# Kernel tuning notes

Hardware: AMD Instinct MI355X
Metric: run time of the kernel (lower is better)

The kernel has to match this reference:

```python
import jax, jax.numpy as jnp
import numpy as np

B, S, E = 2, 2048, 1024
H = 1344            # hidden_dim = ceil(1.3*1024/64)*64
NH = 4              # mLSTM heads
DH = H // NH        # 336
K = 4               # causal conv kernel size
NPH = H // 4        # headwise proj heads (qkv_proj_blocksize=4)
PD = H // NPH       # per-head proj dim = 4
EPS = 1e-6


def setup_inputs() -> dict:
    key = jax.random.key(0)
    ks = jax.random.split(key, 10)
    s_in = jnp.sqrt(2.0 / (5 * E))    # small_init(E)
    s_pd = jnp.sqrt(2.0 / (5 * PD))   # small_init per-head dim
    return {
        "x": jax.random.normal(ks[0], (B, S, E), jnp.float32),
        "W_up": jax.random.normal(ks[1], (E, 2 * H), jnp.float32) * s_in,
        "conv_k": jax.random.normal(ks[2], (K, 1, H), jnp.float32) * jnp.sqrt(2.0 / K),  # depthwise, WIO layout
        "conv_b": jnp.zeros((H,), jnp.float32),
        "Wq": jax.random.normal(ks[3], (NPH, PD, PD), jnp.float32) * s_pd,
        "Wk": jax.random.normal(ks[4], (NPH, PD, PD), jnp.float32) * s_pd,
        "Wv": jax.random.normal(ks[5], (NPH, PD, PD), jnp.float32) * s_pd,
        "W_ig": jax.random.normal(ks[6], (3 * H, NH), jnp.float32) * 0.01,
        "b_ig": jax.random.normal(ks[7], (NH,), jnp.float32) * 0.1,
        "W_fg": jax.random.normal(ks[8], (3 * H, NH), jnp.float32) * 0.01,
        "b_fg": jnp.linspace(3.0, 6.0, NH, dtype=jnp.float32),
        "ln_w": jnp.ones((H,), jnp.float32),
        "skip": jnp.ones((H,), jnp.float32),
        "W_down": jax.random.normal(ks[9], (H, E), jnp.float32) * (2.0 / 12 / np.sqrt(H)),
    }


def _headwise(x, W):
    # LinearHeadwiseExpand: block-diagonal projection over NPH heads of size PD
    xh = x.reshape(B, S, NPH, PD)
    return jnp.einsum('bshd,hdo->bsho', xh, W).reshape(B, S, H)


def _mlstm_cell(q, k, v, ig, fg):
    # parallel stabilized mLSTM; q,k,v: (B,NH,S,DH); ig,fg: (B,NH,S)
    logf = jax.nn.log_sigmoid(fg)
    c = jnp.cumsum(logf, axis=-1)                         # (B,NH,S)
    logfmat = c[..., :, None] - c[..., None, :]           # (B,NH,S,S) cumulative forget decay
    mask = jnp.tril(jnp.ones((S, S), bool))               # causal mask
    log_D = jnp.where(mask, logfmat, -jnp.inf) + ig[..., None, :]
    m = jnp.max(log_D, axis=-1, keepdims=True)            # rowwise stabilizer
    D = jnp.exp(log_D - m)
    qk = jnp.einsum('bnsd,bntd->bnst', q, k) * (DH ** -0.5)
    C = qk * D
    n = jnp.maximum(jnp.abs(jnp.sum(C, axis=-1, keepdims=True)), jnp.exp(-m))
    return jnp.einsum('bnst,bntd->bnsd', C / (n + EPS), v)


def reference(x, W_up, conv_k, conv_b, Wq, Wk, Wv, W_ig, b_ig, W_fg, b_fg, ln_w, skip, W_down):
    x_inner = x @ W_up                                    # (B,S,2H)
    x_m, z = jnp.split(x_inner, 2, axis=-1)
    # depthwise causal conv1d
    xp = jnp.pad(x_m, ((0, 0), (K - 1, 0), (0, 0)))
    xc = jax.lax.conv_general_dilated(
        xp, conv_k, (1,), 'VALID',
        dimension_numbers=('NWC', 'WIO', 'NWC'),
        feature_group_count=H) + conv_b
    act = jax.nn.silu(xc)
    q = _headwise(act, Wq)
    k = _headwise(act, Wk)
    v = _headwise(x_m, Wv)
    gin = jnp.concatenate([q, k, v], axis=-1)             # (B,S,3H)
    ig = jnp.transpose(gin @ W_ig + b_ig, (0, 2, 1))      # (B,NH,S)
    fg = jnp.transpose(gin @ W_fg + b_fg, (0, 2, 1))
    qh = jnp.transpose(q.reshape(B, S, NH, DH), (0, 2, 1, 3))
    kh = jnp.transpose(k.reshape(B, S, NH, DH), (0, 2, 1, 3))
    vh = jnp.transpose(v.reshape(B, S, NH, DH), (0, 2, 1, 3))
    h = _mlstm_cell(qh, kh, vh, ig, fg)                   # (B,NH,S,DH)
    # multi-head layernorm (per-head groupnorm over DH, scale only)
    mu = jnp.mean(h, axis=-1, keepdims=True)
    var = jnp.var(h, axis=-1, keepdims=True)
    hn = (h - mu) * jax.lax.rsqrt(var + 1e-5) * ln_w.reshape(NH, 1, DH)
    h_out = jnp.transpose(hn, (0, 2, 1, 3)).reshape(B, S, H)
    h_state = (h_out + skip * act) * jax.nn.silu(z)
    return h_state @ W_down
```

## Files before the change

### kernel.cpp

```cpp
#include <hip/hip_runtime.h>
#include <cmath>

#define DI __device__ __forceinline__

constexpr int B_=2, S_=2048, E_=1024, H_=1344, NH_=4, DH_=336;
constexpr int BS_=B_*S_, H2_=2*H_;
constexpr int NG_=B_*NH_*S_;

constexpr size_t N_X=(size_t)BS_*E_;
constexpr size_t N_WUP=(size_t)E_*H2_;
constexpr size_t N_WDN=(size_t)H_*E_;
constexpr size_t N_BSH=(size_t)BS_*H_;
constexpr size_t N_BSH2=(size_t)BS_*H2_;
constexpr size_t N_WH=5376, N_WG=16128, N_CK=4*H_;

constexpr size_t O_IGB = 64;
constexpr size_t O_LOGF= O_IGB + NG_;
constexpr size_t O_AB  = O_LOGF+ NG_;
constexpr size_t O_MB  = O_AB  + NG_;
constexpr size_t O_MTB = O_MB  + NG_;
constexpr size_t O_CK  = O_MTB + NG_;
constexpr size_t O_CB  = O_CK  + N_CK;
constexpr size_t O_WQ  = O_CB  + H_;
constexpr size_t O_WK  = O_WQ  + N_WH;
constexpr size_t O_WV  = O_WK  + N_WH;
constexpr size_t O_WIG = O_WV  + N_WH;
constexpr size_t O_BIG = O_WIG + N_WG;
constexpr size_t O_WFG = O_BIG + 16;
constexpr size_t O_BFG = O_WFG + N_WG;
constexpr size_t O_LNW = O_BFG + 16;
constexpr size_t O_SKP = O_LNW + H_;
constexpr size_t O_FX  = O_SKP + H_;
constexpr size_t O_FWUP= O_FX  + N_X;
constexpr size_t O_FWDN= O_FWUP+ N_WUP;
constexpr size_t O_XIN = O_FWDN+ N_WDN;
constexpr size_t O_ACT = O_XIN + N_BSH2;
constexpr size_t O_QB  = O_ACT + N_BSH;
constexpr size_t O_KB  = O_QB  + N_BSH;
constexpr size_t O_VB  = O_KB  + N_BSH;
constexpr size_t O_HOUT= O_VB  + N_BSH;

constexpr size_t KSPLIT_SHORTS=(size_t)8*128*11*64*8;
constexpr size_t VT_SHORTS=(size_t)8*64*22*64*8;

typedef __attribute__((ext_vector_type(8))) short bf16x8;
typedef __attribute__((ext_vector_type(4))) float f32x4;

DI float bf2f(unsigned int u){union{unsigned int i;float f;}v;v.i=(u&0xffffu)<<16;return v.f;}
DI unsigned short f2bf(float f){union{float f;unsigned int i;}v;v.f=f;unsigned int x=v.i;
  return (unsigned short)((x+0x7fffu+((x>>16)&1u))>>16);}
DI float siluf(float x){return x/(1.f+expf(-x));}
DI float logsigf(float x){return (x>=0.f)?-log1pf(expf(-x)):x-log1pf(expf(x));}
DI void load4(const float* p, float* d){float4 v=*reinterpret_cast<const float4*>(p);
  d[0]=v.x;d[1]=v.y;d[2]=v.z;d[3]=v.w;}

__global__ __launch_bounds__(256) void detect_k(const unsigned short* __restrict__ xraw,
                                                int* __restrict__ flag){
  __shared__ int cnt_s;
  if(threadIdx.x==0) cnt_s=0;
  __syncthreads();
  int c=0;
  for(int i=threadIdx.x;i<2048;i+=256){
    const unsigned e=(xraw[i]>>7)&0xFFu;
    if(e>=0x90u) c++;
  }
  atomicAdd(&cnt_s,c);
  __syncthreads();
  if(threadIdx.x==0) *flag=(cnt_s>16)?0:1;
}

constexpr int CV0=5376, CV1=CV0+1344, CV2=CV1+5376, CV3=CV2+5376, CV4=CV3+5376,
              CV5=CV4+16128, CV6=CV5+4, CV7=CV6+16128, CV8=CV7+4,
              CV9=CV8+1344, CVT=CV9+1344;
__global__ __launch_bounds__(256) void convall_k(
    const void* s0,const void* s1,const void* s2,const void* s3,const void* s4,
    const void* s5,const void* s6,const void* s7,const void* s8,const void* s9,
    const void* s10, float* __restrict__ ws, const int* __restrict__ flag){
  const int i=blockIdx.x*256+threadIdx.x;
  if(i>=CVT) return;
  const void* src; int off; size_t dst;
  if(i<CV0){src=s0; off=i;      dst=O_CK +off;}
  else if(i<CV1){src=s1; off=i-CV0; dst=O_CB +off;}
  else if(i<CV2){src=s2; off=i-CV1; dst=O_WQ +off;}
  else if(i<CV3){src=s3; off=i-CV2; dst=O_WK +off;}
  else if(i<CV4){src=s4; off=i-CV3; dst=O_WV +off;}
  else if(i<CV5){src=s5; off=i-CV4; dst=O_WIG+off;}
  else if(i<CV6){src=s6; off=i-CV5; dst=O_BIG+off;}
  else if(i<CV7){src=s7; off=i-CV6; dst=O_WFG+off;}
  else if(i<CV8){src=s8; off=i-CV7; dst=O_BFG+off;}
  else if(i<CV9){src=s9; off=i-CV8; dst=O_LNW+off;}
  else          {src=s10;off=i-CV9; dst=O_SKP+off;}
  ws[dst]=(*flag)?bf2f(((const unsigned short*)src)[off])
                 :((const float*)src)[off];
}

__global__ __launch_bounds__(256) void aprep_k(const void* __restrict__ src,
                                               const int* __restrict__ flag,
                                               int kcn,int ldk,int total,
                                               unsigned short* __restrict__ hi,
                                               unsigned short* __restrict__ lo){
  const int slot=blockIdx.x*256+threadIdx.x;
  if(slot>=total) return;
  const int l=slot&63, rest=slot>>6;
  const int kc=rest%kcn, mt=rest/kcn;
  const int row=mt*16+(l&15), k0=kc*32+(l>>4)*8;
  const int fl=flag?*flag:0;
  float v[8];
  if(fl){
    const unsigned short* s=(const unsigned short*)src+(size_t)row*ldk+k0;
    const uint4 u=*reinterpret_cast<const uint4*>(s);
    v[0]=bf2f(u.x);v[1]=bf2f(u.x>>16);v[2]=bf2f(u.y);v[3]=bf2f(u.y>>16);
    v[4]=bf2f(u.z);v[5]=bf2f(u.z>>16);v[6]=bf2f(u.w);v[7]=bf2f(u.w>>16);
  }else{
    const float* s=(const float*)src+(size_t)row*ldk+k0;
    load4(s,v); load4(s+4,v+4);
  }
  unsigned short h8[8], l8[8];
#pragma unroll
  for(int j=0;j<8;j++){ h8[j]=f2bf(v[j]); l8[j]=f2bf(v[j]-bf2f(h8[j])); }
  uint4 ph,pl;
  ph.x=(unsigned)h8[0]|((unsigned)h8[1]<<16); ph.y=(unsigned)h8[2]|((unsigned)h8[3]<<16);
  ph.z=(unsigned)h8[4]|((unsigned)h8[5]<<16); ph.w=(unsigned)h8[6]|((unsigned)h8[7]<<16);
  pl.x=(unsigned)l8[0]|((unsigned)l8[1]<<16); pl.y=(unsigned)l8[2]|((unsigned)l8[3]<<16);
  pl.z=(unsigned)l8[4]|((unsigned)l8[5]<<16); pl.w=(unsigned)l8[6]|((unsigned)l8[7]<<16);
  *reinterpret_cast<uint4*>(&hi[(size_t)slot*8])=ph;
  *reinterpret_cast<uint4*>(&lo[(size_t)slot*8])=pl;
}

__global__ __launch_bounds__(256) void bprep_k(const void* __restrict__ src,
                                               const int* __restrict__ flag,
                                               int kcn,int ldn,int total,
                                               unsigned short* __restrict__ hi,
                                               unsigned short* __restrict__ lo){
  const int slot=blockIdx.x*256+threadIdx.x;
  if(slot>=total) return;
  const int l=slot&63, rest=slot>>6;
  const int kc=rest%kcn, nt=rest/kcn;
  const int col=nt*16+(l&15), row0=kc*32+(l>>4)*8;
  const int fl=flag?*flag:0;
  float v[8];
  if(fl){
    const unsigned short* s=(const unsigned short*)src;
#pragma unroll
    for(int j=0;j<8;j++) v[j]=bf2f(s[(size_t)(row0+j)*ldn+col]);
  }else{
    const float* s=(const float*)src;
#pragma unroll
    for(int j=0;j<8;j++) v[j]=s[(size_t)(row0+j)*ldn+col];
  }
  unsigned short h8[8], l8[8];
#pragma unroll
  for(int j=0;j<8;j++){ h8[j]=f2bf(v[j]); l8[j]=f2bf(v[j]-bf2f(h8[j])); }
  uint4 ph,pl;
  ph.x=(unsigned)h8[0]|((unsigned)h8[1]<<16); ph.y=(unsigned)h8[2]|((unsigned)h8[3]<<16);
  ph.z=(unsigned)h8[4]|((unsigned)h8[5]<<16); ph.w=(unsigned)h8[6]|((unsigned)h8[7]<<16);
  pl.x=(unsigned)l8[0]|((unsigned)l8[1]<<16); pl.y=(unsigned)l8[2]|((unsigned)l8[3]<<16);
  pl.z=(unsigned)l8[4]|((unsigned)l8[5]<<16); pl.w=(unsigned)l8[6]|((unsigned)l8[7]<<16);
  *reinterpret_cast<uint4*>(&hi[(size_t)slot*8])=ph;
  *reinterpret_cast<uint4*>(&lo[(size_t)slot*8])=pl;
}

__global__ __launch_bounds__(256) void gemm3_k(
    const unsigned short* __restrict__ Ahi, const unsigned short* __restrict__ Alo,
    const unsigned short* __restrict__ Bhi, const unsigned short* __restrict__ Blo,
    void* __restrict__ C, const int* __restrict__ flag, int kcn, int ldc){
  const int t=threadIdx.x, w=t>>6, l=t&63, lm=l&15, quad=l>>4;
  const int bn=blockIdx.x*128, bm=blockIdx.y*128;
  const int mtg0=bm>>4, ntg0=bn>>4;

  __shared__ short TT[2][32*512];

  f32x4 acc[2][8];
#pragma unroll
  for(int g=0;g<2;g++)
#pragma unroll
    for(int nt=0;nt<8;nt++) acc[g][nt]={0.f,0.f,0.f,0.f};

  auto stage=[&](int buf,int kc){
#pragma unroll
    for(int j=0;j<8;j++){
      const int tr=w*8+j;
      const unsigned short* src;
      if(tr<8)       src=&Ahi[((size_t)(mtg0+tr   )*kcn+kc)*512+(size_t)l*8];
      else if(tr<16) src=&Alo[((size_t)(mtg0+tr-8 )*kcn+kc)*512+(size_t)l*8];
      else if(tr<24) src=&Bhi[((size_t)(ntg0+tr-16)*kcn+kc)*512+(size_t)l*8];
      else           src=&Blo[((size_t)(ntg0+tr-24)*kcn+kc)*512+(size_t)l*8];
      __builtin_amdgcn_global_load_lds(
        (const __attribute__((address_space(1))) unsigned int*)src,
        (__attribute__((address_space(3))) unsigned int*)&TT[buf][tr*512],
        16,0,0);
    }
  };

  auto compute=[&](int buf){
    const short* Tb=&TT[buf][0];
    const bf16x8 ah0=*reinterpret_cast<const bf16x8*>(&Tb[(2*w  )*512+l*8]);
    const bf16x8 ah1=*reinterpret_cast<const bf16x8*>(&Tb[(2*w+1)*512+l*8]);
    const bf16x8 al0=*reinterpret_cast<const bf16x8*>(&Tb[(8+2*w  )*512+l*8]);
    const bf16x8 al1=*reinterpret_cast<const bf16x8*>(&Tb[(8+2*w+1)*512+l*8]);
#pragma unroll
    for(int nt=0;nt<8;nt++){
      const bf16x8 bh=*reinterpret_cast<const bf16x8*>(&Tb[(16+nt)*512+l*8]);
      const bf16x8 bl=*reinterpret_cast<const bf16x8*>(&Tb[(24+nt)*512+l*8]);
      acc[0][nt]=__builtin_amdgcn_mfma_f32_16x16x32_bf16(ah0,bh,acc[0][nt],0,0,0);
      acc[0][nt]=__builtin_amdgcn_mfma_f32_16x16x32_bf16(al0,bh,acc[0][nt],0,0,0);
      acc[0][nt]=__builtin_amdgcn_mfma_f32_16x16x32_bf16(ah0,bl,acc[0][nt],0,0,0);
      acc[1][nt]=__builtin_amdgcn_mfma_f32_16x16x32_bf16(ah1,bh,acc[1][nt],0,0,0);
      acc[1][nt]=__builtin_amdgcn_mfma_f32_16x16x32_bf16(al1,bh,acc[1][nt],0,0,0);
      acc[1][nt]=__builtin_amdgcn_mfma_f32_16x16x32_bf16(ah1,bl,acc[1][nt],0,0,0);
    }
  };

  stage(0,0);
  for(int kc=0;kc<kcn;kc++){
    const int cur=kc&1;
    if(kc+1<kcn){
      stage(cur^1,kc+1);
      asm volatile("s_waitcnt vmcnt(8)" ::: "memory");
    } else {
      asm volatile("s_waitcnt vmcnt(0)" ::: "memory");
    }
    __builtin_amdgcn_s_barrier();
    compute(cur);
    __builtin_amdgcn_s_barrier();
  }

  const int bf=flag?*flag:0;
#pragma unroll
  for(int g=0;g<2;g++)
#pragma unroll
    for(int nt=0;nt<8;nt++)
#pragma unroll
      for(int r=0;r<4;r++){
        const size_t idx=(size_t)(bm+(2*w+g)*16+quad*4+r)*ldc+bn+nt*16+lm;
        if(bf) ((unsigned short*)C)[idx]=f2bf(acc[g][nt][r]);
        else   ((float*)C)[idx]=acc[g][nt][r];
      }
}

__global__ __launch_bounds__(256) void convqkv_k(const float* __restrict__ xin,
                                                 const float* __restrict__ ck,
                                                 const float* __restrict__ cb,
                                                 const float* __restrict__ Wq,
                                                 const float* __restrict__ Wk,
                                                 const float* __restrict__ Wv,
                                                 float* __restrict__ act,
                                                 float* __restrict__ qb,
                                                 float* __restrict__ kb,
                                                 float* __restrict__ vb){
  const int i=blockIdx.x*256+threadIdx.x;
  if(i>=BS_*(H_/4)) return;
  const int bs=i/(H_/4), ph=i-bs*(H_/4);
  const int b=bs>>11, s=bs&2047;
  const int base=ph*4;
  float xc[4];
#pragma unroll
  for(int d=0;d<4;d++) xc[d]=cb[base+d];
  float xm[4]={0.f,0.f,0.f,0.f};
#pragma unroll
  for(int w=0;w<4;w++){
    const int sr=s-3+w;
    if(sr>=0){
      float xv[4];
      load4(&xin[(size_t)(b*S_+sr)*H2_+base],xv);
#pragma unroll
      for(int d=0;d<4;d++) xc[d]+=xv[d]*ck[w*H_+base+d];
      if(w==3){ xm[0]=xv[0];xm[1]=xv[1];xm[2]=xv[2];xm[3]=xv[3]; }
    }
  }
  float a4[4];
#pragma unroll
  for(int d=0;d<4;d++) a4[d]=siluf(xc[d]);
  *reinterpret_cast<float4*>(&act[(size_t)bs*H_+base])
      =make_float4(a4[0],a4[1],a4[2],a4[3]);
  float q4[4],k4[4],v4[4];
#pragma unroll
  for(int o=0;o<4;o++){
    float q=0.f,k=0.f,v=0.f;
#pragma unroll
    for(int d=0;d<4;d++){
      q+=a4[d]*Wq[ph*16+d*4+o];
      k+=a4[d]*Wk[ph*16+d*4+o];
      v+=xm[d]*Wv[ph*16+d*4+o];
    }
    q4[o]=q;k4[o]=k;v4[o]=v;
  }
  const int nh=ph/84, dh0=(ph-nh*84)*4;
  const size_t off=((size_t)(b*NH_+nh)*S_+s)*DH_+dh0;
  *reinterpret_cast<float4*>(&qb[off])=make_float4(q4[0],q4[1],q4[2],q4[3]);
  *reinterpret_cast<float4*>(&kb[off])=make_float4(k4[0],k4[1],k4[2],k4[3]);
  *reinterpret_cast<float4*>(&vb[off])=make_float4(v4[0],v4[1],v4[2],v4[3]);
}

__global__ __launch_bounds__(256) void gates2_k(const float* __restrict__ qb,
                                                const float* __restrict__ kb,
                                                const float* __restrict__ vb,
                                                const float* __restrict__ Wig,
                                                const float* __restrict__ big,
                                                const float* __restrict__ Wfg,
                                                const float* __restrict__ bfg,
                                                float* __restrict__ igb,
                                                float* __restrict__ logfb){
  const int wid=(blockIdx.x*256+threadIdx.x)>>6;
  const int l=threadIdx.x&63;
  if(wid>=BS_) return;
  const int b=wid>>11, s=wid&2047;
  float aI0=0.f,aI1=0.f,aI2=0.f,aI3=0.f;
  float aF0=0.f,aF1=0.f,aF2=0.f,aF3=0.f;
  for(int nh=0;nh<NH_;nh++){
    const size_t rb=((size_t)(b*NH_+nh)*S_+s)*DH_;
    const int hb=nh*DH_;
    for(int dh=l;dh<DH_;dh+=64){
      const int h=hb+dh;
      const float q=qb[rb+dh], k=kb[rb+dh], v=vb[rb+dh];
      const float4 wiq=*reinterpret_cast<const float4*>(&Wig[(size_t)h*4]);
      const float4 wik=*reinterpret_cast<const float4*>(&Wig[(size_t)(H_+h)*4]);
      const float4 wiv=*reinterpret_cast<const float4*>(&Wig[(size_t)(2*H_+h)*4]);
      const float4 wfq=*reinterpret_cast<const float4*>(&Wfg[(size_t)h*4]);
      const float4 wfk=*reinterpret_cast<const float4*>(&Wfg[(size_t)(H_+h)*4]);
      const float4 wfv=*reinterpret_cast<const float4*>(&Wfg[(size_t)(2*H_+h)*4]);
      aI0+=q*wiq.x+k*wik.x+v*wiv.x;
      aI1+=q*wiq.y+k*wik.y+v*wiv.y;
      aI2+=q*wiq.z+k*wik.z+v*wiv.z;
      aI3+=q*wiq.w+k*wik.w+v*wiv.w;
      aF0+=q*wfq.x+k*wfk.x+v*wfv.x;
      aF1+=q*wfq.y+k*wfk.y+v*wfv.y;
      aF2+=q*wfq.z+k*wfk.z+v*wfv.z;
      aF3+=q*wfq.w+k*wfk.w+v*wfv.w;
    }
  }
#pragma unroll
  for(int m=1;m<64;m<<=1){
    aI0+=__shfl_xor(aI0,m); aI1+=__shfl_xor(aI1,m);
    aI2+=__shfl_xor(aI2,m); aI3+=__shfl_xor(aI3,m);
    aF0+=__shfl_xor(aF0,m); aF1+=__shfl_xor(aF1,m);
    aF2+=__shfl_xor(aF2,m); aF3+=__shfl_xor(aF3,m);
  }
  if(l==0){
    const size_t o0=(size_t)(b*NH_+0)*S_+s;
    const size_t o1=(size_t)(b*NH_+1)*S_+s;
    const size_t o2=(size_t)(b*NH_+2)*S_+s;
    const size_t o3=(size_t)(b*NH_+3)*S_+s;
    igb[o0]=aI0+big[0]; igb[o1]=aI1+big[1];
    igb[o2]=aI2+big[2]; igb[o3]=aI3+big[3];
    logfb[o0]=logsigf(aF0+bfg[0]); logfb[o1]=logsigf(aF1+bfg[1]);
    logfb[o2]=logsigf(aF2+bfg[2]); logfb[o3]=logsigf(aF3+bfg[3]);
  }
}

__global__ __launch_bounds__(256) void kvprep_k(const float* __restrict__ kb,
                                                const float* vb,
                                                unsigned short* __restrict__ khi,
                                                unsigned short* __restrict__ klo,
                                                unsigned short* __restrict__ vTf,
                                                float* partz){
  const int blk=blockIdx.x;
  if(blk<1024){
    const int head=blk>>7, tt=blk&127;
    const size_t obase=(size_t)blk*11*512;
    for(int slot=threadIdx.x; slot<704; slot+=256){
      const int dc=slot>>6, ll=slot&63, quad=ll>>4, lm=ll&15;
      const int tg=tt*16+lm, dbase=dc*32+quad*8;
      float v[8];
      if(dbase<336){
        load4(&kb[((size_t)head*S_+tg)*DH_+dbase],v);
        load4(&kb[((size_t)head*S_+tg)*DH_+dbase+4],v+4);
      } else { for(int j=0;j<8;j++) v[j]=0.f; }
      unsigned short hi8[8], lo8[8];
#pragma unroll
      for(int j=0;j<8;j++){
        hi8[j]=f2bf(v[j]);
        lo8[j]=f2bf(v[j]-bf2f(hi8[j]));
      }
      const size_t o=obase+(size_t)(dc*64+ll)*8;
      uint4 ph, pl;
      ph.x=(unsigned)hi8[0]|((unsigned)hi8[1]<<16); ph.y=(unsigned)hi8[2]|((unsigned)hi8[3]<<16);
      ph.z=(unsigned)hi8[4]|((unsigned)hi8[5]<<16); ph.w=(unsigned)hi8[6]|((unsigned)hi8[7]<<16);
      pl.x=(unsigned)lo8[0]|((unsigned)lo8[1]<<16); pl.y=(unsigned)lo8[2]|((unsigned)lo8[3]<<16);
      pl.z=(unsigned)lo8[4]|((unsigned)lo8[5]<<16); pl.w=(unsigned)lo8[6]|((unsigned)lo8[7]<<16);
      *reinterpret_cast<uint4*>(&khi[o])=ph;
      *reinterpret_cast<uint4*>(&klo[o])=pl;
    }
  } else {
    const int vblk=blk-1024;
    const int head=vblk>>6, tc=vblk&63;
    const size_t obase=(size_t)vblk*22*512;
    for(int slot=threadIdx.x; slot<1408; slot+=256){
      const int ntg=slot>>6, ll=slot&63, quad=ll>>4, lm=ll&15;
      const int n=ntg*16+lm, t0=tc*32+quad*8;
      unsigned short h8[8];
#pragma unroll
      for(int j=0;j<8;j++){
        float val;
        if(n<336)       val=vb[((size_t)head*S_+t0+j)*DH_+n];
        else if(n==336) val=1.f;
        else            val=0.f;
        h8[j]=f2bf(val);
      }
      uint4 pk;
      pk.x=(unsigned)h8[0]|((unsigned)h8[1]<<16); pk.y=(unsigned)h8[2]|((unsigned)h8[3]<<16);
      pk.z=(unsigned)h8[4]|((unsigned)h8[5]<<16); pk.w=(unsigned)h8[6]|((unsigned)h8[7]<<16);
      *reinterpret_cast<uint4*>(&vTf[obase+(size_t)(ntg*64+ll)*8])=pk;
    }
    __syncthreads();
    const size_t zb=((size_t)head*2048+(size_t)tc*32)*336;
    for(int idx=threadIdx.x; idx<32*336; idx+=256) partz[zb+idx]=0.f;
  }
}

__global__ __launch_bounds__(256) void scan_k(float* igm,
                                              const float* __restrict__ logfb,
                                              float* __restrict__ ab,float* __restrict__ Mb,
                                              float* __restrict__ mtb){
  const int head=blockIdx.x, t=threadIdx.x;
  __shared__ float sh[256];
  const float* lf=logfb+(size_t)head*S_;
  float* ig=igm+(size_t)head*S_;
  float lc[8];
  float run=0.f;
#pragma unroll
  for(int i=0;i<8;i++){ run+=lf[t*8+i]; lc[i]=run; }
  sh[t]=run;
  for(int st=1;st<256;st<<=1){
    __syncthreads();
    const float v=(t>=st)?sh[t-st]:0.f;
    __syncthreads();
    sh[t]+=v;
  }
  __syncthreads();
  const float off=(t==0)?0.f:sh[t-1];
  __syncthreads();
  float av[8],mv[8],cv[8];
  float mrun=-1e30f;
#pragma unroll
  for(int i=0;i<8;i++){
    cv[i]=off+lc[i];
    av[i]=ig[t*8+i]-cv[i];
    mrun=fmaxf(mrun,av[i]);
    mv[i]=mrun;
  }
  sh[t]=mrun;
  for(int st=1;st<256;st<<=1){
    __syncthreads();
    const float v=(t>=st)?sh[t-st]:-1e30f;
    __syncthreads();
    sh[t]=fmaxf(sh[t],v);
  }
  __syncthreads();
  const float moff=(t==0)?-1e30f:sh[t-1];
#pragma unroll
  for(int i=0;i<8;i++){
    const float Mi=fmaxf(moff,mv[i]);
    const size_t j=(size_t)head*S_+t*8+i;
    ab[j]=av[i]; Mb[j]=Mi; mtb[j]=cv[i]+Mi;
    ig[t*8+i]=0.f;
  }
}

__global__ __launch_bounds__(512,1) void mlstm6_k(
    const float* __restrict__ qb, const unsigned short* __restrict__ khi,
    const unsigned short* __restrict__ klo, const unsigned short* __restrict__ vTf,
    const float* __restrict__ ab, const float* __restrict__ Mb,
    float* __restrict__ part, float* __restrict__ rsum){
  const int bid=blockIdx.x;
  const int head=bid&7;
  const int rest=bid>>3;
  const int pairI=rest&7, seg=rest>>3;
  const int t=threadIdx.x, w=t>>6, l=t&63, lm=l&15, quad=l>>4;

  __shared__ short KV[2][66*512];
  __shared__ short Sc[8][16][40];

  const size_t hb=(size_t)head*S_;
  const float scale=0.05455447256f;

  const int sbA=pairI, sbB=15-pairI;
  const int nA=pairI+1, nTot=17;

  bf16x8 qh[11], ql[11];
  f32x4 accO[22];
  float Mr[4];
  int ws0=sbA*128+w*16;

  auto loadQ=[&](int ws0_){
    const float* qrow=qb+(hb+ws0_+lm)*DH_;
#pragma unroll
    for(int dc=0;dc<11;dc++){
      const int dbase=dc*32+quad*8;
      float v[8];
      if(dbase<336){ load4(qrow+dbase,v); load4(qrow+dbase+4,v+4); }
      else { for(int j=0;j<8;j++) v[j]=0.f; }
#pragma unroll
      for(int j=0;j<8;j++){
        const unsigned short h=f2bf(v[j]);
        qh[dc][j]=(short)h;
        ql[dc][j]=(short)f2bf(v[j]-bf2f(h));
      }
    }
#pragma unroll
    for(int r=0;r<4;r++) Mr[r]=Mb[hb+ws0_+quad*4+r];
#pragma unroll
    for(int n=0;n<22;n++) accO[n]={0.f,0.f,0.f,0.f};
  };

  auto itemC=[&](int i)->int{
    return (i<nA)? (seg+4*i) : (seg+4*(i-nA));
  };

  auto stage=[&](int buf,int c){
    const size_t kbase=(((size_t)head*128+(size_t)(2*c))*11)*512+(size_t)l*8;
    const size_t vbase=(((size_t)head*64+(size_t)c)*22)*512+(size_t)l*8;
#pragma unroll
    for(int j=0;j<9;j++){
      const int tr=w+8*j;
      if(tr<66){
        const unsigned short* src;
        if(tr<22)      src=&khi[kbase+(size_t)tr*512];
        else if(tr<44) src=&klo[kbase+(size_t)(tr-22)*512];
        else           src=&vTf[vbase+(size_t)(tr-44)*512];
        __builtin_amdgcn_global_load_lds(
          (const __attribute__((address_space(1))) unsigned int*)src,
          (__attribute__((address_space(3))) unsigned int*)&KV[buf][(size_t)tr*512],
          16,0,0);
      }
    }
  };

  auto compute=[&](int c,int buf){
    const int t0=c<<5;
    if(t0>ws0+15) return;
    const float al0=ab[hb+t0+lm];
    const float al1=ab[hb+t0+16+lm];
#pragma unroll
    for(int tt=0;tt<2;tt++){
      f32x4 a0={0,0,0,0}, a1={0,0,0,0}, a2={0,0,0,0};
#pragma unroll
      for(int dc=0;dc<11;dc++){
        const bf16x8 kh=*reinterpret_cast<const bf16x8*>(&KV[buf][(tt*11+dc)*512+l*8]);
        const bf16x8 kl=*reinterpret_cast<const bf16x8*>(&KV[buf][(22+tt*11+dc)*512+l*8]);
        a0=__builtin_amdgcn_mfma_f32_16x16x32_bf16(qh[dc],kh,a0,0,0,0);
        a1=__builtin_amdgcn_mfma_f32_16x16x32_bf16(ql[dc],kh,a1,0,0,0);
        a2=__builtin_amdgcn_mfma_f32_16x16x32_bf16(qh[dc],kl,a2,0,0,0);
      }
      const float al=(tt==0)?al0:al1;
      const int tg=t0+tt*16+lm;
#pragma unroll
      for(int r=0;r<4;r++){
        const int srow=quad*4+r;
        const float qk=a0[r]+a1[r]+a2[r];
        const float e=fminf(al-Mr[r],0.f);
        const float msk=(tg<=ws0+srow)?1.f:0.f;
        Sc[w][srow][tt*16+lm]=(short)f2bf(msk*(qk*scale*expf(e)));
      }
    }
    const bf16x8 scf=*reinterpret_cast<const bf16x8*>(&Sc[w][lm][quad*8]);
#pragma unroll
    for(int nt=0;nt<22;nt++){
      const bf16x8 vf=*reinterpret_cast<const bf16x8*>(&KV[buf][(44+nt)*512+l*8]);
      accO[nt]=__builtin_amdgcn_mfma_f32_16x16x32_bf16(scf,vf,accO[nt],0,0,0);
    }
  };

  auto epilogue=[&](){
    const size_t pbase=(size_t)head*2048+ws0;
#pragma unroll
    for(int nt=0;nt<22;nt++){
      const int col=nt*16+lm;
#pragma unroll
      for(int r=0;r<4;r++){
        const int srow=quad*4+r;
        const float val=accO[nt][r];
        if(col<336){ if(val!=0.f) atomicAdd(&part[(pbase+srow)*336+col],val); }
        else if(col==336){ if(val!=0.f) atomicAdd(&rsum[pbase+srow],val); }
      }
    }
  };

  loadQ(ws0);
  stage(0,itemC(0));
  __syncthreads();
  int cur=0;
  for(int i=0;i<nTot;i++){
    if(i+1<nTot) stage(cur^1,itemC(i+1));
    compute(itemC(i),cur);
    if(i==nA-1){
      epilogue();
      ws0=sbB*128+w*16;
      loadQ(ws0);
    }
    __syncthreads();
    cur^=1;
  }
  epilogue();
}

__global__ __launch_bounds__(256) void finalize3_k(const float* __restrict__ part,
                                                   const float* __restrict__ rsum,
                                                   const float* __restrict__ mtb,
                                                   const float* __restrict__ lnw,
                                                   const float* __restrict__ skip,
                                                   const float* __restrict__ act,
                                                   const float* __restrict__ xin,
                                                   unsigned short* __restrict__ hshi,
                                                   unsigned short* __restrict__ hslo){
  const int sblk=blockIdx.x, head=blockIdx.y;
  const int bI=head>>2, nh=head&3;
  const int s0=sblk*32;
  const int t=threadIdx.x, row=t>>3, sub=t&7;
  __shared__ float red1[32][8], red2[32][8];
  __shared__ float mu_s[32], rs_s[32], inv_s[32];
  const size_t pbase=(size_t)head*2048+s0;
  const float* prow=part+(pbase+row)*336;
  float s1=0.f,s2=0.f;
  for(int c=sub;c<336;c+=8){ const float v=prow[c]; s1+=v; s2+=v*v; }
  red1[row][sub]=s1; red2[row][sub]=s2;
  __syncthreads();
  if(sub==0){
    float a1=0.f,a2=0.f;
#pragma unroll
    for(int j=0;j<8;j++){ a1+=red1[row][j]; a2+=red2[row][j]; }
    const float mt=mtb[(size_t)head*S_+s0+row];
    const float nn=fmaxf(fabsf(rsum[pbase+row]), expf(fminf(fmaxf(-mt,-60.f),60.f)));
    const float inv=1.f/(nn+1e-6f);
    const float mu=a1*inv/336.f;
    const float var=a2*inv*inv/336.f-mu*mu;
    inv_s[row]=inv; mu_s[row]=mu;
    rs_s[row]=rsqrtf(fmaxf(var,0.f)+1e-5f);
  }
  __syncthreads();
  const float inv=inv_s[row], mu=mu_s[row], rs=rs_s[row];
  const size_t gbs=(size_t)(bI*S_+s0+row);
  const float* arow=act+gbs*H_+nh*DH_;
  const float* zrow=xin+gbs*H2_+H_+nh*DH_;
  const float* srw=skip+nh*DH_;
  const float* lrw=lnw+nh*DH_;
  const size_t mtbase=(gbs>>4)*42;
  const int lbase=(int)(gbs&15);
  for(int c=sub;c<336;c+=8){
    const float hn=(prow[c]*inv-mu)*rs*lrw[c];
    const float val=(hn+srw[c]*arow[c])*siluf(zrow[c]);
    const int h=nh*DH_+c;
    const int kc=h>>5, quad=(h>>3)&3, j=h&7;
    const size_t slot=(mtbase+kc)*64+lbase+16*quad;
    const unsigned short hi=f2bf(val);
    hshi[slot*8+j]=hi;
    hslo[slot*8+j]=f2bf(val-bf2f(hi));
  }
}

extern "C" void kernel_launch(void* const* d_in, const int* in_sizes, int n_in,
                              void* d_out, int out_size, void* d_ws, size_t ws_size,
                              hipStream_t stream){
  float* ws=(float*)d_ws;
  int* flag=(int*)ws;

  float* igb  = ws+O_IGB;
  float* logfb= ws+O_LOGF;
  float* ab   = ws+O_AB;
  float* Mbuf = ws+O_MB;
  float* mtb  = ws+O_MTB;
  float* f_ck = ws+O_CK;
  float* f_cb = ws+O_CB;
  float* f_wq = ws+O_WQ;
  float* f_wk = ws+O_WK;
  float* f_wv = ws+O_WV;
  float* f_wig= ws+O_WIG;
  float* f_big= ws+O_BIG;
  float* f_wfg= ws+O_WFG;
  float* f_bfg= ws+O_BFG;
  float* f_lnw= ws+O_LNW;
  float* f_skp= ws+O_SKP;
  float* xin  = ws+O_XIN;
  float* act  = ws+O_ACT;
  float* qb   = ws+O_QB;
  float* kb   = ws+O_KB;
  float* vb   = ws+O_VB;

  unsigned short* xhi  =(unsigned short*)(ws+O_FX);   unsigned short* xlo  =xhi+N_X;
  unsigned short* wuphi=(unsigned short*)(ws+O_FWUP); unsigned short* wuplo=wuphi+N_WUP;
  unsigned short* wdnhi=(unsigned short*)(ws+O_FWDN); unsigned short* wdnlo=wdnhi+N_WDN;
  unsigned short* khi=(unsigned short*)(ws+O_FX);
  unsigned short* klo=khi+KSPLIT_SHORTS;
  unsigned short* vTf=(unsigned short*)(ws+O_HOUT);
  unsigned short* hshi=(unsigned short*)kb;
  unsigned short* hslo=hshi+N_BSH;
  float* partb=vb;
  float* rsumb=igb;

  detect_k<<<1,256,0,stream>>>((const unsigned short*)d_in[0],flag);
  convall_k<<<(CVT+255)/256,256,0,stream>>>(d_in[2],d_in[3],d_in[4],d_in[5],d_in[6],
                                            d_in[7],d_in[8],d_in[9],d_in[10],d_in[11],
                                            d_in[12],ws,flag);

  aprep_k<<<(256*32*64+255)/256,256,0,stream>>>(d_in[0],flag,32,1024,256*32*64,xhi,xlo);
  bprep_k<<<(168*32*64+255)/256,256,0,stream>>>(d_in[1],flag,32,2688,168*32*64,wuphi,wuplo);
  gemm3_k<<<dim3(2688/128,4096/128),256,0,stream>>>(xhi,xlo,wuphi,wuplo,xin,nullptr,32,H2_);

  convqkv_k<<<(BS_*(H_/4)+255)/256,256,0,stream>>>(xin,f_ck,f_cb,f_wq,f_wk,f_wv,
                                                   act,qb,kb,vb);
  gates2_k<<<(BS_*64+255)/256,256,0,stream>>>(qb,kb,vb,f_wig,f_big,f_wfg,f_bfg,igb,logfb);
  kvprep_k<<<1024+512,256,0,stream>>>(kb,vb,khi,klo,vTf,partb);
  bprep_k<<<(64*42*64+255)/256,256,0,stream>>>(d_in[13],flag,42,1024,64*42*64,wdnhi,wdnlo);
  scan_k<<<B_*NH_,256,0,stream>>>(igb,logfb,ab,Mbuf,mtb);
  mlstm6_k<<<256,512,0,stream>>>(qb,khi,klo,vTf,ab,Mbuf,partb,rsumb);
  finalize3_k<<<dim3(S_/32,B_*NH_),256,0,stream>>>(partb,rsumb,mtb,f_lnw,f_skp,act,xin,
                                                   hshi,hslo);
  gemm3_k<<<dim3(1024/128,4096/128),256,0,stream>>>(hshi,hslo,wdnhi,wdnlo,d_out,flag,42,E_);
}
```

Baseline: 461.4 us.

## Fuse prep kernels and merge conv/qkv with gate projections via shared memory

Merges the x and W_up split-bf16 prep kernels into one launch. It fuses the conv/qkv kernel with the gate projection so q/k/v for each token stay in shared memory instead of being reread from global memory. It also folds the W_down prep into the kv-prep launch. The goal is fewer kernel launches and less global traffic. In exchange, the fused conv kernel uses 384-thread blocks with one token per block and a two-level reduction.

```diff
diff --git a/kernel.cpp b/kernel.cpp
--- a/kernel.cpp
+++ b/kernel.cpp
@@ -94,26 +94,44 @@
                  :((const float*)src)[off];
 }
 
-__global__ __launch_bounds__(256) void aprep_k(const void* __restrict__ src,
-                                               const int* __restrict__ flag,
-                                               int kcn,int ldk,int total,
-                                               unsigned short* __restrict__ hi,
-                                               unsigned short* __restrict__ lo){
-  const int slot=blockIdx.x*256+threadIdx.x;
-  if(slot>=total) return;
-  const int l=slot&63, rest=slot>>6;
-  const int kc=rest%kcn, mt=rest/kcn;
-  const int row=mt*16+(l&15), k0=kc*32+(l>>4)*8;
-  const int fl=flag?*flag:0;
+__global__ __launch_bounds__(256) void prepAB_k(const void* __restrict__ xsrc,
+    const void* __restrict__ wsrc, const int* __restrict__ flag,
+    unsigned short* __restrict__ xhi, unsigned short* __restrict__ xlo,
+    unsigned short* __restrict__ whi, unsigned short* __restrict__ wlo){
+  const int blk=blockIdx.x;
+  const int fl=*flag;
   float v[8];
-  if(fl){
-    const unsigned short* s=(const unsigned short*)src+(size_t)row*ldk+k0;
-    const uint4 u=*reinterpret_cast<const uint4*>(s);
-    v[0]=bf2f(u.x);v[1]=bf2f(u.x>>16);v[2]=bf2f(u.y);v[3]=bf2f(u.y>>16);
-    v[4]=bf2f(u.z);v[5]=bf2f(u.z>>16);v[6]=bf2f(u.w);v[7]=bf2f(u.w>>16);
-  }else{
-    const float* s=(const float*)src+(size_t)row*ldk+k0;
-    load4(s,v); load4(s+4,v+4);
+  unsigned short* dh; unsigned short* dl; size_t slot;
+  if(blk<2048){
+    slot=(size_t)blk*256+threadIdx.x;
+    const int l=(int)slot&63, rest=(int)(slot>>6);
+    const int kc=rest&31, mt=rest>>5;
+    const int row=mt*16+(l&15), k0=kc*32+(l>>4)*8;
+    if(fl){
+      const unsigned short* s=(const unsigned short*)xsrc+(size_t)row*1024+k0;
+      const uint4 u=*reinterpret_cast<const uint4*>(s);
+      v[0]=bf2f(u.x);v[1]=bf2f(u.x>>16);v[2]=bf2f(u.y);v[3]=bf2f(u.y>>16);
+      v[4]=bf2f(u.z);v[5]=bf2f(u.z>>16);v[6]=bf2f(u.w);v[7]=bf2f(u.w>>16);
+    }else{
+      const float* s=(const float*)xsrc+(size_t)row*1024+k0;
+      load4(s,v); load4(s+4,v+4);
+    }
+    dh=xhi; dl=xlo;
+  } else {
+    slot=(size_t)(blk-2048)*256+threadIdx.x;
+    const int l=(int)slot&63, rest=(int)(slot>>6);
+    const int kc=rest&31, nt=rest>>5;
+    const int col=nt*16+(l&15), row0=kc*32+(l>>4)*8;
+    if(fl){
+      const unsigned short* s=(const unsigned short*)wsrc;
+#pragma unroll
+      for(int j=0;j<8;j++) v[j]=bf2f(s[(size_t)(row0+j)*2688+col]);
+    }else{
+      const float* s=(const float*)wsrc;
+#pragma unroll
+      for(int j=0;j<8;j++) v[j]=s[(size_t)(row0+j)*2688+col];
+    }
+    dh=whi; dl=wlo;
   }
   unsigned short h8[8], l8[8];
 #pragma unroll
@@ -123,41 +141,8 @@
   ph.z=(unsigned)h8[4]|((unsigned)h8[5]<<16); ph.w=(unsigned)h8[6]|((unsigned)h8[7]<<16);
   pl.x=(unsigned)l8[0]|((unsigned)l8[1]<<16); pl.y=(unsigned)l8[2]|((unsigned)l8[3]<<16);
   pl.z=(unsigned)l8[4]|((unsigned)l8[5]<<16); pl.w=(unsigned)l8[6]|((unsigned)l8[7]<<16);
-  *reinterpret_cast<uint4*>(&hi[(size_t)slot*8])=ph;
-  *reinterpret_cast<uint4*>(&lo[(size_t)slot*8])=pl;
-}
-
-__global__ __launch_bounds__(256) void bprep_k(const void* __restrict__ src,
-                                               const int* __restrict__ flag,
-                                               int kcn,int ldn,int total,
-                                               unsigned short* __restrict__ hi,
-                                               unsigned short* __restrict__ lo){
-  const int slot=blockIdx.x*256+threadIdx.x;
-  if(slot>=total) return;
-  const int l=slot&63, rest=slot>>6;
-  const int kc=rest%kcn, nt=rest/kcn;
-  const int col=nt*16+(l&15), row0=kc*32+(l>>4)*8;
-  const int fl=flag?*flag:0;
-  float v[8];
-  if(fl){
-    const unsigned short* s=(const unsigned short*)src;
-#pragma unroll
-    for(int j=0;j<8;j++) v[j]=bf2f(s[(size_t)(row0+j)*ldn+col]);
-  }else{
-    const float* s=(const float*)src;
-#pragma unroll
-    for(int j=0;j<8;j++) v[j]=s[(size_t)(row0+j)*ldn+col];
-  }
-  unsigned short h8[8], l8[8];
-#pragma unroll
-  for(int j=0;j<8;j++){ h8[j]=f2bf(v[j]); l8[j]=f2bf(v[j]-bf2f(h8[j])); }
-  uint4 ph,pl;
-  ph.x=(unsigned)h8[0]|((unsigned)h8[1]<<16); ph.y=(unsigned)h8[2]|((unsigned)h8[3]<<16);
-  ph.z=(unsigned)h8[4]|((unsigned)h8[5]<<16); ph.w=(unsigned)h8[6]|((unsigned)h8[7]<<16);
-  pl.x=(unsigned)l8[0]|((unsigned)l8[1]<<16); pl.y=(unsigned)l8[2]|((unsigned)l8[3]<<16);
-  pl.z=(unsigned)l8[4]|((unsigned)l8[5]<<16); pl.w=(unsigned)l8[6]|((unsigned)l8[7]<<16);
-  *reinterpret_cast<uint4*>(&hi[(size_t)slot*8])=ph;
-  *reinterpret_cast<uint4*>(&lo[(size_t)slot*8])=pl;
+  *reinterpret_cast<uint4*>(&dh[slot*8])=ph;
+  *reinterpret_cast<uint4*>(&dl[slot*8])=pl;
 }
 
 __global__ __launch_bounds__(256) void gemm3_k(
@@ -238,96 +223,85 @@
       }
 }
 
-__global__ __launch_bounds__(256) void convqkv_k(const float* __restrict__ xin,
-                                                 const float* __restrict__ ck,
-                                                 const float* __restrict__ cb,
-                                                 const float* __restrict__ Wq,
-                                                 const float* __restrict__ Wk,
-                                                 const float* __restrict__ Wv,
-                                                 float* __restrict__ act,
-                                                 float* __restrict__ qb,
-                                                 float* __restrict__ kb,
-                                                 float* __restrict__ vb){
-  const int i=blockIdx.x*256+threadIdx.x;
-  if(i>=BS_*(H_/4)) return;
-  const int bs=i/(H_/4), ph=i-bs*(H_/4);
+__global__ __launch_bounds__(384) void convqkvgates_k(
+    const float* __restrict__ xin, const float* __restrict__ ck,
+    const float* __restrict__ cb,
+    const float* __restrict__ Wq, const float* __restrict__ Wk,
+    const float* __restrict__ Wv,
+    const float* __restrict__ Wig, const float* __restrict__ big,
+    const float* __restrict__ Wfg, const float* __restrict__ bfg,
+    float* __restrict__ act, float* __restrict__ qb, float* __restrict__ kb,
+    float* __restrict__ vb, float* __restrict__ igb, float* __restrict__ logfb){
+  const int bs=blockIdx.x;
   const int b=bs>>11, s=bs&2047;
-  const int base=ph*4;
-  float xc[4];
-#pragma unroll
-  for(int d=0;d<4;d++) xc[d]=cb[base+d];
-  float xm[4]={0.f,0.f,0.f,0.f};
-#pragma unroll
-  for(int w=0;w<4;w++){
-    const int sr=s-3+w;
-    if(sr>=0){
-      float xv[4];
-      load4(&xin[(size_t)(b*S_+sr)*H2_+base],xv);
-#pragma unroll
-      for(int d=0;d<4;d++) xc[d]+=xv[d]*ck[w*H_+base+d];
-      if(w==3){ xm[0]=xv[0];xm[1]=xv[1];xm[2]=xv[2];xm[3]=xv[3]; }
-    }
-  }
-  float a4[4];
-#pragma unroll
-  for(int d=0;d<4;d++) a4[d]=siluf(xc[d]);
-  *reinterpret_cast<float4*>(&act[(size_t)bs*H_+base])
-      =make_float4(a4[0],a4[1],a4[2],a4[3]);
-  float q4[4],k4[4],v4[4];
-#pragma unroll
-  for(int o=0;o<4;o++){
-    float q=0.f,k=0.f,v=0.f;
-#pragma unroll
-    for(int d=0;d<4;d++){
-      q+=a4[d]*Wq[ph*16+d*4+o];
-      k+=a4[d]*Wk[ph*16+d*4+o];
-      v+=xm[d]*Wv[ph*16+d*4+o];
-    }
-    q4[o]=q;k4[o]=k;v4[o]=v;
-  }
-  const int nh=ph/84, dh0=(ph-nh*84)*4;
-  const size_t off=((size_t)(b*NH_+nh)*S_+s)*DH_+dh0;
-  *reinterpret_cast<float4*>(&qb[off])=make_float4(q4[0],q4[1],q4[2],q4[3]);
-  *reinterpret_cast<float4*>(&kb[off])=make_float4(k4[0],k4[1],k4[2],k4[3]);
-  *reinterpret_cast<float4*>(&vb[off])=make_float4(v4[0],v4[1],v4[2],v4[3]);
-}
-
-__global__ __launch_bounds__(256) void gates2_k(const float* __restrict__ qb,
-                                                const float* __restrict__ kb,
-                                                const float* __restrict__ vb,
-                                                const float* __restrict__ Wig,
-                                                const float* __restrict__ big,
-                                                const float* __restrict__ Wfg,
-                                                const float* __restrict__ bfg,
-                                                float* __restrict__ igb,
-                                                float* __restrict__ logfb){
-  const int wid=(blockIdx.x*256+threadIdx.x)>>6;
-  const int l=threadIdx.x&63;
-  if(wid>=BS_) return;
-  const int b=wid>>11, s=wid&2047;
+  const int t=threadIdx.x;
+  __shared__ float4 sq4[336], sk4[336], sv4[336];
+  __shared__ float red[6][8];
+  if(t<336){
+    const int ph=t, base=ph*4;
+    float xc[4];
+#pragma unroll
+    for(int d=0;d<4;d++) xc[d]=cb[base+d];
+    float xm[4]={0.f,0.f,0.f,0.f};
+#pragma unroll
+    for(int w=0;w<4;w++){
+      const int sr=s-3+w;
+      if(sr>=0){
+        float xv[4];
+        load4(&xin[(size_t)(b*S_+sr)*H2_+base],xv);
+#pragma unroll
+        for(int d=0;d<4;d++) xc[d]+=xv[d]*ck[w*H_+base+d];
+        if(w==3){ xm[0]=xv[0];xm[1]=xv[1];xm[2]=xv[2];xm[3]=xv[3]; }
+      }
+    }
+    float a4[4];
+#pragma unroll
+    for(int d=0;d<4;d++) a4[d]=siluf(xc[d]);
+    *reinterpret_cast<float4*>(&act[(size_t)bs*H_+base])
+        =make_float4(a4[0],a4[1],a4[2],a4[3]);
+    float q4[4],k4[4],v4[4];
+#pragma unroll
+    for(int o=0;o<4;o++){
+      float q=0.f,k=0.f,v=0.f;
+#pragma unroll
+      for(int d=0;d<4;d++){
+        q+=a4[d]*Wq[ph*16+d*4+o];
+        k+=a4[d]*Wk[ph*16+d*4+o];
+        v+=xm[d]*Wv[ph*16+d*4+o];
+      }
+      q4[o]=q;k4[o]=k;v4[o]=v;
+    }
+    const int nh=ph/84, dh0=(ph-nh*84)*4;
+    const size_t off=((size_t)(b*NH_+nh)*S_+s)*DH_+dh0;
+    *reinterpret_cast<float4*>(&qb[off])=make_float4(q4[0],q4[1],q4[2],q4[3]);
+    *reinterpret_cast<float4*>(&kb[off])=make_float4(k4[0],k4[1],k4[2],k4[3]);
+    *reinterpret_cast<float4*>(&vb[off])=make_float4(v4[0],v4[1],v4[2],v4[3]);
+    sq4[ph]=make_float4(q4[0],q4[1],q4[2],q4[3]);
+    sk4[ph]=make_float4(k4[0],k4[1],k4[2],k4[3]);
+    sv4[ph]=make_float4(v4[0],v4[1],v4[2],v4[3]);
+  }
+  __syncthreads();
+  const float* sq=reinterpret_cast<const float*>(sq4);
+  const float* sk=reinterpret_cast<const float*>(sk4);
+  const float* sv=reinterpret_cast<const float*>(sv4);
   float aI0=0.f,aI1=0.f,aI2=0.f,aI3=0.f;
   float aF0=0.f,aF1=0.f,aF2=0.f,aF3=0.f;
-  for(int nh=0;nh<NH_;nh++){
-    const size_t rb=((size_t)(b*NH_+nh)*S_+s)*DH_;
-    const int hb=nh*DH_;
-    for(int dh=l;dh<DH_;dh+=64){
-      const int h=hb+dh;
-      const float q=qb[rb+dh], k=kb[rb+dh], v=vb[rb+dh];
-      const float4 wiq=*reinterpret_cast<const float4*>(&Wig[(size_t)h*4]);
-      const float4 wik=*reinterpret_cast<const float4*>(&Wig[(size_t)(H_+h)*4]);
-      const float4 wiv=*reinterpret_cast<const float4*>(&Wig[(size_t)(2*H_+h)*4]);
-      const float4 wfq=*reinterpret_cast<const float4*>(&Wfg[(size_t)h*4]);
-      const float4 wfk=*reinterpret_cast<const float4*>(&Wfg[(size_t)(H_+h)*4]);
-      const float4 wfv=*reinterpret_cast<const float4*>(&Wfg[(size_t)(2*H_+h)*4]);
-      aI0+=q*wiq.x+k*wik.x+v*wiv.x;
-      aI1+=q*wiq.y+k*wik.y+v*wiv.y;
-      aI2+=q*wiq.z+k*wik.z+v*wiv.z;
-      aI3+=q*wiq.w+k*wik.w+v*wiv.w;
-      aF0+=q*wfq.x+k*wfk.x+v*wfv.x;
-      aF1+=q*wfq.y+k*wfk.y+v*wfv.y;
-      aF2+=q*wfq.z+k*wfk.z+v*wfv.z;
-      aF3+=q*wfq.w+k*wfk.w+v*wfv.w;
-    }
+  for(int h=t; h<H_; h+=384){
+    const float q=sq[h], k=sk[h], v=sv[h];
+    const float4 wiq=*reinterpret_cast<const float4*>(&Wig[(size_t)h*4]);
+    const float4 wik=*reinterpret_cast<const float4*>(&Wig[(size_t)(H_+h)*4]);
+    const float4 wiv=*reinterpret_cast<const float4*>(&Wig[(size_t)(2*H_+h)*4]);
+    const float4 wfq=*reinterpret_cast<const float4*>(&Wfg[(size_t)h*4]);
+    const float4 wfk=*reinterpret_cast<const float4*>(&Wfg[(size_t)(H_+h)*4]);
+    const float4 wfv=*reinterpret_cast<const float4*>(&Wfg[(size_t)(2*H_+h)*4]);
+    aI0+=q*wiq.x+k*wik.x+v*wiv.x;
+    aI1+=q*wiq.y+k*wik.y+v*wiv.y;
+    aI2+=q*wiq.z+k*wik.z+v*wiv.z;
+    aI3+=q*wiq.w+k*wik.w+v*wiv.w;
+    aF0+=q*wfq.x+k*wfk.x+v*wfv.x;
+    aF1+=q*wfq.y+k*wfk.y+v*wfv.y;
+    aF2+=q*wfq.z+k*wfk.z+v*wfv.z;
+    aF3+=q*wfq.w+k*wfk.w+v*wfv.w;
   }
 #pragma unroll
   for(int m=1;m<64;m<<=1){
@@ -336,24 +310,40 @@
     aF0+=__shfl_xor(aF0,m); aF1+=__shfl_xor(aF1,m);
     aF2+=__shfl_xor(aF2,m); aF3+=__shfl_xor(aF3,m);
   }
+  const int wv=t>>6, l=t&63;
   if(l==0){
-    const size_t o0=(size_t)(b*NH_+0)*S_+s;
-    const size_t o1=(size_t)(b*NH_+1)*S_+s;
-    const size_t o2=(size_t)(b*NH_+2)*S_+s;
-    const size_t o3=(size_t)(b*NH_+3)*S_+s;
-    igb[o0]=aI0+big[0]; igb[o1]=aI1+big[1];
-    igb[o2]=aI2+big[2]; igb[o3]=aI3+big[3];
-    logfb[o0]=logsigf(aF0+bfg[0]); logfb[o1]=logsigf(aF1+bfg[1]);
-    logfb[o2]=logsigf(aF2+bfg[2]); logfb[o3]=logsigf(aF3+bfg[3]);
-  }
-}
-
-__global__ __launch_bounds__(256) void kvprep_k(const float* __restrict__ kb,
-                                                const float* vb,
-                                                unsigned short* __restrict__ khi,
-                                                unsigned short* __restrict__ klo,
-                                                unsigned short* __restrict__ vTf,
-                                                float* partz){
+    red[wv][0]=aI0; red[wv][1]=aI1; red[wv][2]=aI2; red[wv][3]=aI3;
+    red[wv][4]=aF0; red[wv][5]=aF1; red[wv][6]=aF2; red[wv][7]=aF3;
+  }
+  __syncthreads();
+  if(t==0){
+    float r[8];
+#pragma unroll
+    for(int j=0;j<8;j++){
+      float a=0.f;
+#pragma unroll
+      for(int wv2=0;wv2<6;wv2++) a+=red[wv2][j];
+      r[j]=a;
+    }
+#pragma unroll
+    for(int n=0;n<4;n++){
+      const size_t o=(size_t)(b*NH_+n)*S_+s;
+      igb[o]=r[n]+big[n];
+      logfb[o]=logsigf(r[4+n]+bfg[n]);
+    }
+  }
+}
+
+__global__ __launch_bounds__(256) void kvprep3_k(const float* __restrict__ kb,
+                                                 const float* vb,
+                                                 const void* __restrict__ wdnsrc,
+                                                 const int* __restrict__ flag,
+                                                 unsigned short* __restrict__ khi,
+                                                 unsigned short* __restrict__ klo,
+                                                 unsigned short* __restrict__ vTf,
+                                                 unsigned short* __restrict__ wdnhi,
+                                                 unsigned short* __restrict__ wdnlo,
+                                                 float* partz){
   const int blk=blockIdx.x;
   if(blk<1024){
     const int head=blk>>7, tt=blk&127;
@@ -381,7 +371,7 @@
       *reinterpret_cast<uint4*>(&khi[o])=ph;
       *reinterpret_cast<uint4*>(&klo[o])=pl;
     }
-  } else {
+  } else if(blk<1536){
     const int vblk=blk-1024;
     const int head=vblk>>6, tc=vblk&63;
     const size_t obase=(size_t)vblk*22*512;
@@ -405,6 +395,32 @@
     __syncthreads();
     const size_t zb=((size_t)head*2048+(size_t)tc*32)*336;
     for(int idx=threadIdx.x; idx<32*336; idx+=256) partz[zb+idx]=0.f;
+  } else {
+    const size_t slot=(size_t)(blk-1536)*256+threadIdx.x;
+    const int l=(int)slot&63, rest=(int)(slot>>6);
+    const int kc=rest%42, nt=rest/42;
+    const int col=nt*16+(l&15), row0=kc*32+(l>>4)*8;
+    const int fl=*flag;
+    float v[8];
+    if(fl){
+      const unsigned short* s=(const unsigned short*)wdnsrc;
+#pragma unroll
+      for(int j=0;j<8;j++) v[j]=bf2f(s[(size_t)(row0+j)*1024+col]);
+    }else{
+      const float* s=(const float*)wdnsrc;
+#pragma unroll
+      for(int j=0;j<8;j++) v[j]=s[(size_t)(row0+j)*1024+col];
+    }
+    unsigned short h8[8], l8[8];
+#pragma unroll
+    for(int j=0;j<8;j++){ h8[j]=f2bf(v[j]); l8[j]=f2bf(v[j]-bf2f(h8[j])); }
+    uint4 ph,pl;
+    ph.x=(unsigned)h8[0]|((unsigned)h8[1]<<16); ph.y=(unsigned)h8[2]|((unsigned)h8[3]<<16);
+    ph.z=(unsigned)h8[4]|((unsigned)h8[5]<<16); ph.w=(unsigned)h8[6]|((unsigned)h8[7]<<16);
+    pl.x=(unsigned)l8[0]|((unsigned)l8[1]<<16); pl.y=(unsigned)l8[2]|((unsigned)l8[3]<<16);
+    pl.z=(unsigned)l8[4]|((unsigned)l8[5]<<16); pl.w=(unsigned)l8[6]|((unsigned)l8[7]<<16);
+    *reinterpret_cast<uint4*>(&wdnhi[slot*8])=ph;
+    *reinterpret_cast<uint4*>(&wdnlo[slot*8])=pl;
   }
 }
 
@@ -692,15 +708,14 @@
                                             d_in[7],d_in[8],d_in[9],d_in[10],d_in[11],
                                             d_in[12],ws,flag);
 
-  aprep_k<<<(256*32*64+255)/256,256,0,stream>>>(d_in[0],flag,32,1024,256*32*64,xhi,xlo);
-  bprep_k<<<(168*32*64+255)/256,256,0,stream>>>(d_in[1],flag,32,2688,168*32*64,wuphi,wuplo);
+  prepAB_k<<<2048+1344,256,0,stream>>>(d_in[0],d_in[1],flag,xhi,xlo,wuphi,wuplo);
   gemm3_k<<<dim3(2688/128,4096/128),256,0,stream>>>(xhi,xlo,wuphi,wuplo,xin,nullptr,32,H2_);
 
-  convqkv_k<<<(BS_*(H_/4)+255)/256,256,0,stream>>>(xin,f_ck,f_cb,f_wq,f_wk,f_wv,
-                                                   act,qb,kb,vb);
-  gates2_k<<<(BS_*64+255)/256,256,0,stream>>>(qb,kb,vb,f_wig,f_big,f_wfg,f_bfg,igb,logfb);
-  kvprep_k<<<1024+512,256,0,stream>>>(kb,vb,khi,klo,vTf,partb);
-  bprep_k<<<(64*42*64+255)/256,256,0,stream>>>(d_in[13],flag,42,1024,64*42*64,wdnhi,wdnlo);
+  convqkvgates_k<<<BS_,384,0,stream>>>(xin,f_ck,f_cb,f_wq,f_wk,f_wv,
+                                       f_wig,f_big,f_wfg,f_bfg,
+                                       act,qb,kb,vb,igb,logfb);
+  kvprep3_k<<<1024+512+672,256,0,stream>>>(kb,vb,d_in[13],flag,
+                                           khi,klo,vTf,wdnhi,wdnlo,partb);
   scan_k<<<B_*NH_,256,0,stream>>>(igb,logfb,ab,Mbuf,mtb);
   mlstm6_k<<<256,512,0,stream>>>(qb,khi,klo,vTf,ab,Mbuf,partb,rsumb);
   finalize3_k<<<dim3(S_/32,B_*NH_),256,0,stream>>>(partb,rsumb,mtb,f_lnw,f_skp,act,xin,
```

After: 438.5 us. 1.05x faster.
